# Kernel optimization log

Hardware: AMD Instinct MI355X
Metric: run time of the kernel (lower is better)

Reference implementation:

```python
import jax, jax.numpy as jnp
import numpy as np

IN_FEATURES = 512
OUT_FEATURES = 1024
ALPHA = 1.0
BATCH = 8192


def setup_inputs() -> dict:
    key = jax.random.key(0)
    kx, kw = jax.random.split(key)
    x = jax.random.normal(kx, (BATCH, IN_FEATURES), dtype=jnp.float32)
    # xavier_uniform for weight of shape (out, in): limit = sqrt(6/(fan_in+fan_out))
    limit = float(np.sqrt(6.0 / (IN_FEATURES + OUT_FEATURES)))
    weight = jax.random.uniform(kw, (OUT_FEATURES, IN_FEATURES), dtype=jnp.float32,
                                minval=-limit, maxval=limit)
    return {"x": x, "weight": weight}


def reference(x, weight):
    # dist: [B, K]
    x_sq = jnp.sum(x * x, axis=1, keepdims=True)            # [B, 1]
    w_sq = jnp.sum(weight * weight, axis=1)                  # [K]
    dist = x_sq + w_sq[None, :] - 2.0 * jnp.einsum('bd,kd->bk', x, weight)
    dist = jnp.maximum(dist, 0.0)
    # Student-t kernel soft assignment
    q = (1.0 + dist / ALPHA) ** (-(ALPHA + 1.0) / 2.0)       # [B, K]
    q = q / jnp.sum(q, axis=1, keepdims=True)                # row-normalize
    return q
```

## Files before the change

kernel.cpp:

```cpp
#include <hip/hip_runtime.h>
#include <hip/hip_bf16.h>

#define BATCH 8192
#define DIM   512
#define NCL   1024
#define ROWS  32
#define BK    32
#define NCH   (DIM / BK)
#define NWAVE 16

typedef __bf16 bf16x8 __attribute__((ext_vector_type(8)));
typedef float  f32x4  __attribute__((ext_vector_type(4)));

__device__ __forceinline__ unsigned short f2bf(float f) {
  union { float f; unsigned u; } v; v.f = f;
  unsigned r = v.u + 0x7fffu + ((v.u >> 16) & 1u);
  return (unsigned short)(r >> 16);
}
__device__ __forceinline__ unsigned pk(float a, float b) {
  return (unsigned)f2bf(a) | ((unsigned)f2bf(b) << 16);
}

__global__ __launch_bounds__(256) void prep_w(const float* __restrict__ w,
                                              __hip_bfloat16* __restrict__ wck,
                                              float* __restrict__ wsq) {
  int k    = blockIdx.x * 4 + (threadIdx.x >> 6);
  int lane = threadIdx.x & 63;
  const float4* wrow = (const float4*)(w + (size_t)k * DIM);
  float4 a = wrow[lane * 2 + 0];
  float4 b = wrow[lane * 2 + 1];
  float s = a.x*a.x + a.y*a.y + a.z*a.z + a.w*a.w
          + b.x*b.x + b.y*b.y + b.z*b.z + b.w*b.w;
  #pragma unroll
  for (int m = 32; m >= 1; m >>= 1) s += __shfl_xor(s, m, 64);
  if (lane == 0) wsq[k] = s;
  int c = lane >> 2;
  int j = (lane & 3) * 8;
  uint4 p = { pk(a.x, a.y), pk(a.z, a.w), pk(b.x, b.y), pk(b.z, b.w) };
  *(uint4*)(wck + ((size_t)c * NCL + k) * BK + j) = p;
}

__global__ __launch_bounds__(1024, 4) void fused(const float* __restrict__ x,
                                                 const __hip_bfloat16* __restrict__ wck,
                                                 const float* __restrict__ wsq,
                                                 float* __restrict__ out) {
  __shared__ __align__(16) __hip_bfloat16 xs2[NCH * 2 * 512];
  __shared__ float wsq_s[NCL];
  __shared__ float xqp[NWAVE][33];
  __shared__ float xsq_s[ROWS];
  __shared__ float red[ROWS][NWAVE + 1];
  __shared__ float rowtot[ROWS];

  const int tid = threadIdx.x;
  const int r0  = blockIdx.x * ROWS;

  const int wave = tid >> 6;
  const int lane = tid & 63;
  const int m16  = lane & 15;
  const int quad = lane >> 4;
  const int col0 = wave * 64;

  bf16x8 bcur[4];
  {
    const __hip_bfloat16* wp0 = wck + (size_t)(col0 + m16) * BK + quad * 8;
    #pragma unroll
    for (int ct = 0; ct < 4; ++ct)
      bcur[ct] = *(const bf16x8*)(wp0 + ct * (16 * BK));
  }

  {
    int row = tid & 31;
    int seg = tid >> 5;
    int c = seg >> 1, h = seg & 1;
    int rt = row >> 4, m = row & 15;
    const float4* src = (const float4*)(x + (size_t)(r0 + row) * DIM + seg * 16);
    float4 v0 = src[0], v1 = src[1], v2 = src[2], v3 = src[3];
    float ss = v0.x*v0.x + v0.y*v0.y + v0.z*v0.z + v0.w*v0.w
             + v1.x*v1.x + v1.y*v1.y + v1.z*v1.z + v1.w*v1.w
             + v2.x*v2.x + v2.y*v2.y + v2.z*v2.z + v2.w*v2.w
             + v3.x*v3.x + v3.y*v3.y + v3.z*v3.z + v3.w*v3.w;
    __hip_bfloat16* base = xs2 + (c * 2 + rt) * 512 + m * 8;
    uint4 p0 = { pk(v0.x, v0.y), pk(v0.z, v0.w), pk(v1.x, v1.y), pk(v1.z, v1.w) };
    uint4 p1 = { pk(v2.x, v2.y), pk(v2.z, v2.w), pk(v3.x, v3.y), pk(v3.z, v3.w) };
    *(uint4*)(base + (h * 2 + 0) * 128) = p0;
    *(uint4*)(base + (h * 2 + 1) * 128) = p1;
    ss += __shfl_xor(ss, 32, 64);
    if (lane < 32) xqp[wave][row] = ss;
    wsq_s[tid] = wsq[tid];
  }

  f32x4 acc[2][4];
  #pragma unroll
  for (int rt = 0; rt < 2; ++rt)
    #pragma unroll
    for (int ct = 0; ct < 4; ++ct)
      acc[rt][ct] = (f32x4){0.f, 0.f, 0.f, 0.f};

  __syncthreads();
  if (tid < ROWS) {
    float t = 0.f;
    #pragma unroll
    for (int w2 = 0; w2 < NWAVE; ++w2) t += xqp[w2][tid];
    xsq_s[tid] = t;
  }
  __syncthreads();

  bf16x8 a0 = *(const bf16x8*)(xs2 + 0 * 512 + lane * 8);
  bf16x8 a1 = *(const bf16x8*)(xs2 + 1 * 512 + lane * 8);

  #pragma unroll
  for (int c = 0; c < NCH; ++c) {
    bf16x8 bnx[4], na0, na1;
    if (c + 1 < NCH) {
      const __hip_bfloat16* wp = wck + ((size_t)(c + 1) * NCL + col0 + m16) * BK + quad * 8;
      #pragma unroll
      for (int ct = 0; ct < 4; ++ct)
        bnx[ct] = *(const bf16x8*)(wp + ct * (16 * BK));
      na0 = *(const bf16x8*)(xs2 + ((c + 1) * 2 + 0) * 512 + lane * 8);
      na1 = *(const bf16x8*)(xs2 + ((c + 1) * 2 + 1) * 512 + lane * 8);
    }
    #pragma unroll
    for (int ct = 0; ct < 4; ++ct) {
      acc[0][ct] = __builtin_amdgcn_mfma_f32_16x16x32_bf16(a0, bcur[ct], acc[0][ct], 0, 0, 0);
      acc[1][ct] = __builtin_amdgcn_mfma_f32_16x16x32_bf16(a1, bcur[ct], acc[1][ct], 0, 0, 0);
    }
    if (c + 1 < NCH) {
      #pragma unroll
      for (int ct = 0; ct < 4; ++ct) bcur[ct] = bnx[ct];
      a0 = na0; a1 = na1;
    }
  }

  float part[2][4];
  #pragma unroll
  for (int rt = 0; rt < 2; ++rt)
    #pragma unroll
    for (int i = 0; i < 4; ++i) part[rt][i] = 0.f;

  #pragma unroll
  for (int rt = 0; rt < 2; ++rt) {
    float xq[4];
    #pragma unroll
    for (int i = 0; i < 4; ++i) xq[i] = xsq_s[rt * 16 + quad * 4 + i];
    #pragma unroll
    for (int ct = 0; ct < 4; ++ct) {
      float wq = wsq_s[col0 + ct * 16 + m16];
      #pragma unroll
      for (int i = 0; i < 4; ++i) {
        float dist = fmaxf(xq[i] + wq - 2.f * acc[rt][ct][i], 0.f);
        float qu = 1.f / (1.f + dist);
        acc[rt][ct][i] = qu;
        part[rt][i] += qu;
      }
    }
  }
  #pragma unroll
  for (int rt = 0; rt < 2; ++rt)
    #pragma unroll
    for (int i = 0; i < 4; ++i) {
      float s = part[rt][i];
      s += __shfl_xor(s, 1, 64);
      s += __shfl_xor(s, 2, 64);
      s += __shfl_xor(s, 4, 64);
      s += __shfl_xor(s, 8, 64);
      part[rt][i] = s;
    }
  if (m16 == 0) {
    #pragma unroll
    for (int rt = 0; rt < 2; ++rt)
      #pragma unroll
      for (int i = 0; i < 4; ++i)
        red[rt * 16 + quad * 4 + i][wave] = part[rt][i];
  }
  __syncthreads();
  if (tid < ROWS) {
    float t = 0.f;
    #pragma unroll
    for (int w2 = 0; w2 < NWAVE; ++w2) t += red[tid][w2];
    rowtot[tid] = 1.f / t;
  }
  __syncthreads();
  #pragma unroll
  for (int rt = 0; rt < 2; ++rt) {
    #pragma unroll
    for (int i = 0; i < 4; ++i) {
      int r = rt * 16 + quad * 4 + i;
      float inv = rowtot[r];
      float* orow = out + (size_t)(r0 + r) * NCL + col0 + m16;
      #pragma unroll
      for (int ct = 0; ct < 4; ++ct)
        orow[ct * 16] = acc[rt][ct][i] * inv;
    }
  }
}

extern "C" void kernel_launch(void* const* d_in, const int* in_sizes, int n_in,
                              void* d_out, int out_size, void* d_ws, size_t ws_size,
                              hipStream_t stream) {
  const float* x = (const float*)d_in[0];
  const float* w = (const float*)d_in[1];
  __hip_bfloat16* wck = (__hip_bfloat16*)d_ws;
  float* wsq = (float*)((char*)d_ws + (size_t)NCH * NCL * BK * 2);
  float* out = (float*)d_out;

  hipLaunchKernelGGL(prep_w, dim3(NCL / 4), dim3(256), 0, stream, w, wck, wsq);
  hipLaunchKernelGGL(fused, dim3(BATCH / ROWS), dim3(1024), 0, stream, x, wck, wsq, out);
}
```

Before: 97.68 us.

## Cut block barriers via shuffle row norms, LDS atomics, and staggered K-chunk order

Each 32-lane half-wave now reads one full x row, so the row squared norm is reduced with wave shuffles and written directly, which removes a barrier and a serial reduction pass. Row sums of the soft assignments are accumulated with shared-memory atomicAdd instead of a per-wave table followed by a serial reduction, which removes another barrier. Each wave also starts its K-chunk loop at a different chunk, spreading LDS and L2 accesses across banks and lines. The row-major x load changes the global coalescing pattern, and the atomics make floating-point summation order nondeterministic.

```diff
diff --git a/kernel.cpp b/kernel.cpp
--- a/kernel.cpp
+++ b/kernel.cpp
@@ -46,10 +46,8 @@
                                                  float* __restrict__ out) {
   __shared__ __align__(16) __hip_bfloat16 xs2[NCH * 2 * 512];
   __shared__ float wsq_s[NCL];
-  __shared__ float xqp[NWAVE][33];
   __shared__ float xsq_s[ROWS];
-  __shared__ float red[ROWS][NWAVE + 1];
-  __shared__ float rowtot[ROWS];
+  __shared__ float rowsum[ROWS];
 
   const int tid = threadIdx.x;
   const int r0  = blockIdx.x * ROWS;
@@ -59,22 +57,23 @@
   const int m16  = lane & 15;
   const int quad = lane >> 4;
   const int col0 = wave * 64;
+  const int c0   = wave;
 
   bf16x8 bcur[4];
   {
-    const __hip_bfloat16* wp0 = wck + (size_t)(col0 + m16) * BK + quad * 8;
+    const __hip_bfloat16* wp0 = wck + ((size_t)c0 * NCL + col0 + m16) * BK + quad * 8;
     #pragma unroll
     for (int ct = 0; ct < 4; ++ct)
       bcur[ct] = *(const bf16x8*)(wp0 + ct * (16 * BK));
   }
 
   {
-    int row = tid & 31;
-    int seg = tid >> 5;
+    int row = tid >> 5;
+    int seg = tid & 31;
     int c = seg >> 1, h = seg & 1;
     int rt = row >> 4, m = row & 15;
-    const float4* src = (const float4*)(x + (size_t)(r0 + row) * DIM + seg * 16);
-    float4 v0 = src[0], v1 = src[1], v2 = src[2], v3 = src[3];
+    const f32x4* src = (const f32x4*)(x + (size_t)(r0 + row) * DIM + seg * 16);
+    f32x4 v0 = src[0], v1 = src[1], v2 = src[2], v3 = src[3];
     float ss = v0.x*v0.x + v0.y*v0.y + v0.z*v0.z + v0.w*v0.w
              + v1.x*v1.x + v1.y*v1.y + v1.z*v1.z + v1.w*v1.w
              + v2.x*v2.x + v2.y*v2.y + v2.z*v2.z + v2.w*v2.w
@@ -84,9 +83,14 @@
     uint4 p1 = { pk(v2.x, v2.y), pk(v2.z, v2.w), pk(v3.x, v3.y), pk(v3.z, v3.w) };
     *(uint4*)(base + (h * 2 + 0) * 128) = p0;
     *(uint4*)(base + (h * 2 + 1) * 128) = p1;
-    ss += __shfl_xor(ss, 32, 64);
-    if (lane < 32) xqp[wave][row] = ss;
+    ss += __shfl_xor(ss, 1, 64);
+    ss += __shfl_xor(ss, 2, 64);
+    ss += __shfl_xor(ss, 4, 64);
+    ss += __shfl_xor(ss, 8, 64);
+    ss += __shfl_xor(ss, 16, 64);
+    if ((lane & 31) == 0) xsq_s[row] = ss;
     wsq_s[tid] = wsq[tid];
+    if (tid < ROWS) rowsum[tid] = 0.f;
   }
 
   f32x4 acc[2][4];
@@ -97,51 +101,40 @@
       acc[rt][ct] = (f32x4){0.f, 0.f, 0.f, 0.f};
 
   __syncthreads();
-  if (tid < ROWS) {
-    float t = 0.f;
-    #pragma unroll
-    for (int w2 = 0; w2 < NWAVE; ++w2) t += xqp[w2][tid];
-    xsq_s[tid] = t;
-  }
-  __syncthreads();
 
-  bf16x8 a0 = *(const bf16x8*)(xs2 + 0 * 512 + lane * 8);
-  bf16x8 a1 = *(const bf16x8*)(xs2 + 1 * 512 + lane * 8);
+  bf16x8 a0 = *(const bf16x8*)(xs2 + (c0 * 2 + 0) * 512 + lane * 8);
+  bf16x8 a1 = *(const bf16x8*)(xs2 + (c0 * 2 + 1) * 512 + lane * 8);
 
   #pragma unroll
-  for (int c = 0; c < NCH; ++c) {
-    bf16x8 bnx[4], na0, na1;
-    if (c + 1 < NCH) {
-      const __hip_bfloat16* wp = wck + ((size_t)(c + 1) * NCL + col0 + m16) * BK + quad * 8;
+  for (int it = 0; it < NCH; ++it) {
+    bf16x8 bnx[4], a0n, a1n;
+    if (it + 1 < NCH) {
+      int cn = (c0 + it + 1) & (NCH - 1);
+      const __hip_bfloat16* wp = wck + ((size_t)cn * NCL + col0 + m16) * BK + quad * 8;
       #pragma unroll
       for (int ct = 0; ct < 4; ++ct)
         bnx[ct] = *(const bf16x8*)(wp + ct * (16 * BK));
-      na0 = *(const bf16x8*)(xs2 + ((c + 1) * 2 + 0) * 512 + lane * 8);
-      na1 = *(const bf16x8*)(xs2 + ((c + 1) * 2 + 1) * 512 + lane * 8);
+      a0n = *(const bf16x8*)(xs2 + (cn * 2 + 0) * 512 + lane * 8);
+      a1n = *(const bf16x8*)(xs2 + (cn * 2 + 1) * 512 + lane * 8);
     }
     #pragma unroll
     for (int ct = 0; ct < 4; ++ct) {
       acc[0][ct] = __builtin_amdgcn_mfma_f32_16x16x32_bf16(a0, bcur[ct], acc[0][ct], 0, 0, 0);
       acc[1][ct] = __builtin_amdgcn_mfma_f32_16x16x32_bf16(a1, bcur[ct], acc[1][ct], 0, 0, 0);
     }
-    if (c + 1 < NCH) {
+    if (it + 1 < NCH) {
+      a0 = a0n; a1 = a1n;
       #pragma unroll
       for (int ct = 0; ct < 4; ++ct) bcur[ct] = bnx[ct];
-      a0 = na0; a1 = na1;
     }
   }
 
   float part[2][4];
   #pragma unroll
-  for (int rt = 0; rt < 2; ++rt)
-    #pragma unroll
-    for (int i = 0; i < 4; ++i) part[rt][i] = 0.f;
-
-  #pragma unroll
   for (int rt = 0; rt < 2; ++rt) {
     float xq[4];
     #pragma unroll
-    for (int i = 0; i < 4; ++i) xq[i] = xsq_s[rt * 16 + quad * 4 + i];
+    for (int i = 0; i < 4; ++i) { xq[i] = xsq_s[rt * 16 + quad * 4 + i]; part[rt][i] = 0.f; }
     #pragma unroll
     for (int ct = 0; ct < 4; ++ct) {
       float wq = wsq_s[col0 + ct * 16 + m16];
@@ -170,14 +163,7 @@
     for (int rt = 0; rt < 2; ++rt)
       #pragma unroll
       for (int i = 0; i < 4; ++i)
-        red[rt * 16 + quad * 4 + i][wave] = part[rt][i];
-  }
-  __syncthreads();
-  if (tid < ROWS) {
-    float t = 0.f;
-    #pragma unroll
-    for (int w2 = 0; w2 < NWAVE; ++w2) t += red[tid][w2];
-    rowtot[tid] = 1.f / t;
+        atomicAdd(&rowsum[rt * 16 + quad * 4 + i], part[rt][i]);
   }
   __syncthreads();
   #pragma unroll
@@ -185,7 +171,7 @@
     #pragma unroll
     for (int i = 0; i < 4; ++i) {
       int r = rt * 16 + quad * 4 + i;
-      float inv = rowtot[r];
+      float inv = 1.f / rowsum[r];
       float* orow = out + (size_t)(r0 + r) * NCL + col0 + m16;
       #pragma unroll
       for (int ct = 0; ct < 4; ++ct)
```

Result: no change. 96.55 us (-1.2%).
